# Performance work log

Measured on AMD Instinct MI355X. Metric: run time of the kernel, lower is better.

## Reference

```python
import jax, jax.numpy as jnp
import numpy as np

B = 8192          # batch
LATENT = 32       # latent_dim
H = 64            # hidden_size
SEQ_LEN = 180
NUM_CLASSES = 6
IN = 2            # GRU input size (zeros) / output features


def setup_inputs() -> dict:
    key = jax.random.key(0)
    ks = jax.random.split(key, 12)
    s_fc = 1.0 / np.sqrt(LATENT + H)
    s_rnn = 1.0 / np.sqrt(H)
    return {
        "z": jax.random.normal(ks[0], (B, LATENT), dtype=jnp.float32),
        "labels": jax.random.randint(ks[1], (B,), 0, NUM_CLASSES),
        "embed_w": jax.random.normal(ks[2], (NUM_CLASSES, H), dtype=jnp.float32),
        "fc_w": jax.random.uniform(ks[3], (H, LATENT + H), jnp.float32, -s_fc, s_fc),
        "fc_b": jax.random.uniform(ks[4], (H,), jnp.float32, -s_fc, s_fc),
        "w_ih": jax.random.uniform(ks[5], (3 * H, IN), jnp.float32, -s_rnn, s_rnn),
        "w_hh": jax.random.uniform(ks[6], (3 * H, H), jnp.float32, -s_rnn, s_rnn),
        "b_ih": jax.random.uniform(ks[7], (3 * H,), jnp.float32, -s_rnn, s_rnn),
        "b_hh": jax.random.uniform(ks[8], (3 * H,), jnp.float32, -s_rnn, s_rnn),
        "out_w": jax.random.uniform(ks[9], (IN, H), jnp.float32, -s_rnn, s_rnn),
        "out_b": jax.random.uniform(ks[10], (IN,), jnp.float32, -s_rnn, s_rnn),
    }


def reference(z, labels, embed_w, fc_w, fc_b, w_ih, w_hh, b_ih, b_hh, out_w, out_b):
    # h0 = tanh(fc([z, embed(labels)]))  -> [B, H]
    cond = embed_w[labels]
    h0 = jnp.tanh(jnp.concatenate([z, cond], axis=1) @ fc_w.T + fc_b)

    # GRU input is all zeros, so the input-side gates are constant per step:
    # gi = x_t @ w_ih.T + b_ih = b_ih  (kept faithful to torch GRU math)
    i_r, i_z, i_n = jnp.split(b_ih, 3)

    def step(h, _):
        gh = h @ w_hh.T + b_hh                      # [B, 3H]
        h_r, h_z, h_n = jnp.split(gh, 3, axis=-1)
        r = jax.nn.sigmoid(i_r + h_r)
        zg = jax.nn.sigmoid(i_z + h_z)
        n = jnp.tanh(i_n + r * h_n)
        h_new = (1.0 - zg) * n + zg * h
        return h_new, h_new

    _, hs = jax.lax.scan(step, h0, None, length=SEQ_LEN)  # [S, B, H]
    # out linear: [B, S, 2]
    return jnp.einsum("sbh,oh->bso", hs, out_w) + out_b
```

## Files before the change

### kernel.cpp

```cpp
#include <hip/hip_runtime.h>

#define NB     8192
#define HDIM   64
#define SEQ    180
#define MT     16
#define SB     72
#define XSP    100

typedef __bf16 bf16x8 __attribute__((ext_vector_type(8)));
typedef __bf16 bf16x4 __attribute__((ext_vector_type(4)));
typedef float  f32x4  __attribute__((ext_vector_type(4)));

#define L2E 1.44269504088896340736f

__device__ __forceinline__ float tanh_f(float x) {
    float e = __builtin_amdgcn_exp2f((2.0f * L2E) * x);
    return 1.0f - 2.0f * __builtin_amdgcn_rcpf(1.0f + e);
}

#define MFMA __builtin_amdgcn_mfma_f32_16x16x32_bf16

__global__ __launch_bounds__(256) void gru_all(
        const float* __restrict__ z, const int* __restrict__ labels,
        const float* __restrict__ embed_w, const float* __restrict__ fc_w,
        const float* __restrict__ fc_b, const float* __restrict__ w_hh,
        const float* __restrict__ b_ih, const float* __restrict__ b_hh,
        const float* __restrict__ out_w, const float* __restrict__ out_b,
        float* __restrict__ out) {
    __shared__ __align__(16) __bf16 hbuf[2][MT * SB];
    __shared__ __align__(16) float  xs[MT * XSP];

    const int t = threadIdx.x;
    const int w = t >> 6;
    const int l = t & 63;
    const int q = l >> 4;
    const int n16 = l & 15;
    const int jg = 16 * w + n16;
    const int jb = 16 * w + 4 * q;
    const int bbase = blockIdx.x * MT;

    for (int c = t; c < MT * 24; c += 256) {
        int m = c / 24, kk = (c % 24) * 4;
        f32x4 v;
        if (kk < 32) v = *(const f32x4*)(z + (size_t)(bbase + m) * 32 + kk);
        else         v = *(const f32x4*)(embed_w + labels[bbase + m] * 64 + (kk - 32));
        *(f32x4*)(xs + m * XSP + kk) = v;
    }

    bf16x8 whi[3][2];
#pragma unroll
    for (int g = 0; g < 3; ++g) {
        const float* pr = w_hh + (g * 64 + jg) * HDIM;
#pragma unroll
        for (int ks = 0; ks < 2; ++ks) {
            const float* p = pr + ks * 32 + q * 8;
            f32x4 va = *(const f32x4*)(p);
            f32x4 vb = *(const f32x4*)(p + 4);
#pragma unroll
            for (int j2 = 0; j2 < 4; ++j2) {
                whi[g][ks][j2]     = (__bf16)va[j2];
                whi[g][ks][4 + j2] = (__bf16)vb[j2];
            }
        }
    }

    bf16x8 obhi[2];
#pragma unroll
    for (int ks = 0; ks < 2; ++ks) {
        f32x4 va = {0.f, 0.f, 0.f, 0.f}, vb = {0.f, 0.f, 0.f, 0.f};
        if (n16 < 2) {
            va = *(const f32x4*)(out_w + n16 * 64 + ks * 32 + q * 8);
            vb = *(const f32x4*)(out_w + n16 * 64 + ks * 32 + q * 8 + 4);
        }
#pragma unroll
        for (int j2 = 0; j2 < 4; ++j2) {
            obhi[ks][j2]     = (__bf16)va[j2];
            obhi[ks][4 + j2] = (__bf16)vb[j2];
        }
    }
    const f32x4 obias = (q == 0) ? f32x4{out_b[0], out_b[1], 0.f, 0.f}
                                 : f32x4{0.f, 0.f, 0.f, 0.f};
    const f32x4 kZ = {0.f, 0.f, 0.f, 0.f};
    const f32x4 one4 = {1.f, 1.f, 1.f, 1.f};

    const bool ostorer = (q == 0) && ((n16 >> 2) == w);

    const f32x4 bihR = *(const f32x4*)(b_ih + jb);
    const f32x4 bhhR = *(const f32x4*)(b_hh + jb);
    const f32x4 bihZ = *(const f32x4*)(b_ih + 64 + jb);
    const f32x4 bhhZ = *(const f32x4*)(b_hh + 64 + jb);
    const f32x4 cR4 = (bihR + bhhR) * (-L2E);
    const f32x4 cZ4 = (bihZ + bhhZ) * (-L2E);
    const f32x4 bn4 = *(const f32x4*)(b_hh + 128 + jb);
    const f32x4 cN4 = (*(const f32x4*)(b_ih + 128 + jb)) * (2.0f * L2E);

    const int rdoff = n16 * SB + q * 8;
    const int wboff = n16 * SB + jb;
    float* opb = out + (size_t)(bbase + n16) * (SEQ * 2);

    __syncthreads();

    f32x4 hprev;
    {
        f32x4 a = *(const f32x4*)(fc_b + jb);
        for (int kc = 0; kc < 24; ++kc) {
            f32x4 xv = *(const f32x4*)(xs + n16 * XSP + kc * 4);
#pragma unroll
            for (int r = 0; r < 4; ++r) {
                f32x4 wv = *(const f32x4*)(fc_w + (size_t)(jb + r) * 96 + kc * 4);
                a[r] += wv[0] * xv[0] + wv[1] * xv[1] + wv[2] * xv[2] + wv[3] * xv[3];
            }
        }
        bf16x4 hp;
#pragma unroll
        for (int r = 0; r < 4; ++r) {
            hprev[r] = tanh_f(a[r]);
            hp[r] = (__bf16)hprev[r];
        }
        *(bf16x4*)(hbuf[0] + wboff) = hp;
    }
    __syncthreads();

    if ((blockIdx.x >> 8) & 1) __builtin_amdgcn_s_sleep(8);

    for (int u = 0; u < SEQ / 4; ++u) {
#pragma unroll
        for (int s = 0; s < 4; ++s) {
            const int p = s & 1;
            const __bf16* Hh = hbuf[p];
            __bf16* Nh = hbuf[1 - p];

            bf16x8 b0 = *(const bf16x8*)(Hh + rdoff);
            bf16x8 b1 = *(const bf16x8*)(Hh + rdoff + 32);

            f32x4 aR, aZ, aN;
            aR = MFMA(whi[0][0], b0, kZ, 0, 0, 0);
            aZ = MFMA(whi[1][0], b0, kZ, 0, 0, 0);
            aN = MFMA(whi[2][0], b0, kZ, 0, 0, 0);
            aR = MFMA(whi[0][1], b1, aR, 0, 0, 0);
            aZ = MFMA(whi[1][1], b1, aZ, 0, 0, 0);
            aN = MFMA(whi[2][1], b1, aN, 0, 0, 0);

            f32x4 tR = aR * (-L2E) + cR4;
            f32x4 tZ = aZ * (-L2E) + cZ4;
            f32x4 eR, eZ;
#pragma unroll
            for (int r = 0; r < 4; ++r) {
                eR[r] = __builtin_amdgcn_exp2f(tR[r]);
                eZ[r] = __builtin_amdgcn_exp2f(tZ[r]);
            }
            eR = eR + one4;
            eZ = eZ + one4;
            f32x4 rg, zg;
#pragma unroll
            for (int r = 0; r < 4; ++r) {
                rg[r] = __builtin_amdgcn_rcpf(eR[r]);
                zg[r] = __builtin_amdgcn_rcpf(eZ[r]);
            }
            f32x4 mm = aN + bn4;
            f32x4 tN = (rg * mm) * (2.0f * L2E) + cN4;
            f32x4 eN;
#pragma unroll
            for (int r = 0; r < 4; ++r) eN[r] = __builtin_amdgcn_exp2f(tN[r]);
            eN = eN + one4;
            f32x4 dd;
#pragma unroll
            for (int r = 0; r < 4; ++r) dd[r] = __builtin_amdgcn_rcpf(eN[r]);
            f32x4 ng = dd * (-2.0f) + one4;
            f32x4 hn = zg * (hprev - ng) + ng;
            hprev = hn;
            bf16x4 hp;
#pragma unroll
            for (int r = 0; r < 4; ++r) hp[r] = (__bf16)hn[r];
            *(bf16x4*)(Nh + wboff) = hp;

            {
                f32x4 o = obias;
                o = MFMA(obhi[0], b0, o, 0, 0, 0);
                o = MFMA(obhi[1], b1, o, 0, 0, 0);
                if ((u | s) != 0 && ostorer)
                    *(float2*)(opb + (8 * u + 2 * s - 2)) = make_float2(o[0], o[1]);
            }

            __syncthreads();
        }
    }

    {
        const __bf16* Hh = hbuf[0];
        bf16x8 b0 = *(const bf16x8*)(Hh + rdoff);
        bf16x8 b1 = *(const bf16x8*)(Hh + rdoff + 32);
        f32x4 o = obias;
        o = MFMA(obhi[0], b0, o, 0, 0, 0);
        o = MFMA(obhi[1], b1, o, 0, 0, 0);
        if (ostorer)
            *(float2*)(opb + (SEQ - 1) * 2) = make_float2(o[0], o[1]);
    }
}

extern "C" void kernel_launch(void* const* d_in, const int* in_sizes, int n_in,
                              void* d_out, int out_size, void* d_ws, size_t ws_size,
                              hipStream_t stream) {
    (void)in_sizes; (void)n_in; (void)out_size; (void)d_ws; (void)ws_size;
    const float* z       = (const float*)d_in[0];
    const int*   labels  = (const int*)d_in[1];
    const float* embed_w = (const float*)d_in[2];
    const float* fc_w    = (const float*)d_in[3];
    const float* fc_b    = (const float*)d_in[4];
    const float* w_hh    = (const float*)d_in[6];
    const float* b_ih    = (const float*)d_in[7];
    const float* b_hh    = (const float*)d_in[8];
    const float* out_w   = (const float*)d_in[9];
    const float* out_b   = (const float*)d_in[10];
    float* out = (float*)d_out;

    gru_all<<<NB / MT, 256, 0, stream>>>(z, labels, embed_w, fc_w, fc_b,
                                         w_hh, b_ih, b_hh, out_w, out_b, out);
}
```

Before: 172.7 us.

## Interleave two independent batch tiles per block to hide recurrence latency

Each block now processes two 16-row batch tiles, issuing the MFMAs and gate epilogues for both recurrences together so one tile's latency hides behind the other's work. This halves the grid and the number of per-step barriers per batch row. The blockIdx-based s_sleep stagger is removed. In exchange, register pressure rises and each CU gets fewer blocks, so less parallelism comes from separate wavefronts.

```diff
diff --git a/kernel.cpp b/kernel.cpp
--- a/kernel.cpp
+++ b/kernel.cpp
@@ -1,9 +1,10 @@
 #include <hip/hip_runtime.h>
 
-#define NB     8192
+#define NBATCH 8192
 #define HDIM   64
 #define SEQ    180
 #define MT     16
+#define NC     2
 #define SB     72
 #define XSP    100
 
@@ -19,6 +20,43 @@
 }
 
 #define MFMA __builtin_amdgcn_mfma_f32_16x16x32_bf16
+
+__device__ __forceinline__ f32x4 gru_epi(f32x4 aR, f32x4 aZ, f32x4 aN,
+        f32x4 cR4, f32x4 cZ4, f32x4 bn4, f32x4 cN4, f32x4 one4,
+        f32x4 hprev, __bf16* Nh, int wboff) {
+    f32x4 tR = aR * (-L2E) + cR4;
+    f32x4 tZ = aZ * (-L2E) + cZ4;
+    f32x4 eR, eZ;
+#pragma unroll
+    for (int r = 0; r < 4; ++r) {
+        eR[r] = __builtin_amdgcn_exp2f(tR[r]);
+        eZ[r] = __builtin_amdgcn_exp2f(tZ[r]);
+    }
+    eR = eR + one4;
+    eZ = eZ + one4;
+    f32x4 rg, zg;
+#pragma unroll
+    for (int r = 0; r < 4; ++r) {
+        rg[r] = __builtin_amdgcn_rcpf(eR[r]);
+        zg[r] = __builtin_amdgcn_rcpf(eZ[r]);
+    }
+    f32x4 mm = aN + bn4;
+    f32x4 tN = (rg * mm) * (2.0f * L2E) + cN4;
+    f32x4 eN;
+#pragma unroll
+    for (int r = 0; r < 4; ++r) eN[r] = __builtin_amdgcn_exp2f(tN[r]);
+    eN = eN + one4;
+    f32x4 dd;
+#pragma unroll
+    for (int r = 0; r < 4; ++r) dd[r] = __builtin_amdgcn_rcpf(eN[r]);
+    f32x4 ng = dd * (-2.0f) + one4;
+    f32x4 hn = zg * (hprev - ng) + ng;
+    bf16x4 hp;
+#pragma unroll
+    for (int r = 0; r < 4; ++r) hp[r] = (__bf16)hn[r];
+    *(bf16x4*)(Nh + wboff) = hp;
+    return hn;
+}
 
 __global__ __launch_bounds__(256) void gru_all(
         const float* __restrict__ z, const int* __restrict__ labels,
@@ -27,8 +65,8 @@
         const float* __restrict__ b_ih, const float* __restrict__ b_hh,
         const float* __restrict__ out_w, const float* __restrict__ out_b,
         float* __restrict__ out) {
-    __shared__ __align__(16) __bf16 hbuf[2][MT * SB];
-    __shared__ __align__(16) float  xs[MT * XSP];
+    __shared__ __align__(16) __bf16 hbuf[NC][2][MT * SB];
+    __shared__ __align__(16) float  xs[NC * MT * XSP];
 
     const int t = threadIdx.x;
     const int w = t >> 6;
@@ -37,9 +75,9 @@
     const int n16 = l & 15;
     const int jg = 16 * w + n16;
     const int jb = 16 * w + 4 * q;
-    const int bbase = blockIdx.x * MT;
-
-    for (int c = t; c < MT * 24; c += 256) {
+    const int bbase = blockIdx.x * (NC * MT);
+
+    for (int c = t; c < NC * MT * 24; c += 256) {
         int m = c / 24, kk = (c % 24) * 4;
         f32x4 v;
         if (kk < 32) v = *(const f32x4*)(z + (size_t)(bbase + m) * 32 + kk);
@@ -96,105 +134,97 @@
 
     const int rdoff = n16 * SB + q * 8;
     const int wboff = n16 * SB + jb;
-    float* opb = out + (size_t)(bbase + n16) * (SEQ * 2);
+    float* opbA = out + (size_t)(bbase + n16) * (SEQ * 2);
+    float* opbB = out + (size_t)(bbase + MT + n16) * (SEQ * 2);
 
     __syncthreads();
 
-    f32x4 hprev;
+    f32x4 hpA, hpB;
     {
-        f32x4 a = *(const f32x4*)(fc_b + jb);
+        f32x4 aA = *(const f32x4*)(fc_b + jb);
+        f32x4 aB = aA;
         for (int kc = 0; kc < 24; ++kc) {
-            f32x4 xv = *(const f32x4*)(xs + n16 * XSP + kc * 4);
+            f32x4 xvA = *(const f32x4*)(xs + n16 * XSP + kc * 4);
+            f32x4 xvB = *(const f32x4*)(xs + (MT + n16) * XSP + kc * 4);
 #pragma unroll
             for (int r = 0; r < 4; ++r) {
                 f32x4 wv = *(const f32x4*)(fc_w + (size_t)(jb + r) * 96 + kc * 4);
-                a[r] += wv[0] * xv[0] + wv[1] * xv[1] + wv[2] * xv[2] + wv[3] * xv[3];
+                aA[r] += wv[0] * xvA[0] + wv[1] * xvA[1] + wv[2] * xvA[2] + wv[3] * xvA[3];
+                aB[r] += wv[0] * xvB[0] + wv[1] * xvB[1] + wv[2] * xvB[2] + wv[3] * xvB[3];
             }
         }
-        bf16x4 hp;
+        bf16x4 ha, hb;
 #pragma unroll
         for (int r = 0; r < 4; ++r) {
-            hprev[r] = tanh_f(a[r]);
-            hp[r] = (__bf16)hprev[r];
-        }
-        *(bf16x4*)(hbuf[0] + wboff) = hp;
+            hpA[r] = tanh_f(aA[r]); ha[r] = (__bf16)hpA[r];
+            hpB[r] = tanh_f(aB[r]); hb[r] = (__bf16)hpB[r];
+        }
+        *(bf16x4*)(hbuf[0][0] + wboff) = ha;
+        *(bf16x4*)(hbuf[1][0] + wboff) = hb;
     }
     __syncthreads();
 
-    if ((blockIdx.x >> 8) & 1) __builtin_amdgcn_s_sleep(8);
-
-    for (int u = 0; u < SEQ / 4; ++u) {
-#pragma unroll
-        for (int s = 0; s < 4; ++s) {
-            const int p = s & 1;
-            const __bf16* Hh = hbuf[p];
-            __bf16* Nh = hbuf[1 - p];
-
-            bf16x8 b0 = *(const bf16x8*)(Hh + rdoff);
-            bf16x8 b1 = *(const bf16x8*)(Hh + rdoff + 32);
-
-            f32x4 aR, aZ, aN;
-            aR = MFMA(whi[0][0], b0, kZ, 0, 0, 0);
-            aZ = MFMA(whi[1][0], b0, kZ, 0, 0, 0);
-            aN = MFMA(whi[2][0], b0, kZ, 0, 0, 0);
-            aR = MFMA(whi[0][1], b1, aR, 0, 0, 0);
-            aZ = MFMA(whi[1][1], b1, aZ, 0, 0, 0);
-            aN = MFMA(whi[2][1], b1, aN, 0, 0, 0);
-
-            f32x4 tR = aR * (-L2E) + cR4;
-            f32x4 tZ = aZ * (-L2E) + cZ4;
-            f32x4 eR, eZ;
-#pragma unroll
-            for (int r = 0; r < 4; ++r) {
-                eR[r] = __builtin_amdgcn_exp2f(tR[r]);
-                eZ[r] = __builtin_amdgcn_exp2f(tZ[r]);
+    for (int u = 0; u < SEQ / 2; ++u) {
+#pragma unroll
+        for (int s = 0; s < 2; ++s) {
+            const __bf16* HA = hbuf[0][s];
+            __bf16*       NA = hbuf[0][s ^ 1];
+            const __bf16* HB = hbuf[1][s];
+            __bf16*      NhB = hbuf[1][s ^ 1];
+
+            bf16x8 a0 = *(const bf16x8*)(HA + rdoff);
+            bf16x8 a1 = *(const bf16x8*)(HA + rdoff + 32);
+            bf16x8 c0 = *(const bf16x8*)(HB + rdoff);
+            bf16x8 c1 = *(const bf16x8*)(HB + rdoff + 32);
+
+            f32x4 ArA = MFMA(whi[0][0], a0, kZ, 0, 0, 0);
+            f32x4 AzA = MFMA(whi[1][0], a0, kZ, 0, 0, 0);
+            f32x4 AnA = MFMA(whi[2][0], a0, kZ, 0, 0, 0);
+            f32x4 ArB = MFMA(whi[0][0], c0, kZ, 0, 0, 0);
+            f32x4 AzB = MFMA(whi[1][0], c0, kZ, 0, 0, 0);
+            f32x4 AnB = MFMA(whi[2][0], c0, kZ, 0, 0, 0);
+            ArA = MFMA(whi[0][1], a1, ArA, 0, 0, 0);
+            AzA = MFMA(whi[1][1], a1, AzA, 0, 0, 0);
+            AnA = MFMA(whi[2][1], a1, AnA, 0, 0, 0);
+            ArB = MFMA(whi[0][1], c1, ArB, 0, 0, 0);
+            AzB = MFMA(whi[1][1], c1, AzB, 0, 0, 0);
+            AnB = MFMA(whi[2][1], c1, AnB, 0, 0, 0);
+
+            {
+                f32x4 oA = obias;
+                oA = MFMA(obhi[0], a0, oA, 0, 0, 0);
+                oA = MFMA(obhi[1], a1, oA, 0, 0, 0);
+                f32x4 oB = obias;
+                oB = MFMA(obhi[0], c0, oB, 0, 0, 0);
+                oB = MFMA(obhi[1], c1, oB, 0, 0, 0);
+                if ((u | s) != 0 && ostorer) {
+                    *(float2*)(opbA + (4 * u + 2 * s - 2)) = make_float2(oA[0], oA[1]);
+                    *(float2*)(opbB + (4 * u + 2 * s - 2)) = make_float2(oB[0], oB[1]);
+                }
             }
-            eR = eR + one4;
-            eZ = eZ + one4;
-            f32x4 rg, zg;
-#pragma unroll
-            for (int r = 0; r < 4; ++r) {
-                rg[r] = __builtin_amdgcn_rcpf(eR[r]);
-                zg[r] = __builtin_amdgcn_rcpf(eZ[r]);
-            }
-            f32x4 mm = aN + bn4;
-            f32x4 tN = (rg * mm) * (2.0f * L2E) + cN4;
-            f32x4 eN;
-#pragma unroll
-            for (int r = 0; r < 4; ++r) eN[r] = __builtin_amdgcn_exp2f(tN[r]);
-            eN = eN + one4;
-            f32x4 dd;
-#pragma unroll
-            for (int r = 0; r < 4; ++r) dd[r] = __builtin_amdgcn_rcpf(eN[r]);
-            f32x4 ng = dd * (-2.0f) + one4;
-            f32x4 hn = zg * (hprev - ng) + ng;
-            hprev = hn;
-            bf16x4 hp;
-#pragma unroll
-            for (int r = 0; r < 4; ++r) hp[r] = (__bf16)hn[r];
-            *(bf16x4*)(Nh + wboff) = hp;
-
-            {
-                f32x4 o = obias;
-                o = MFMA(obhi[0], b0, o, 0, 0, 0);
-                o = MFMA(obhi[1], b1, o, 0, 0, 0);
-                if ((u | s) != 0 && ostorer)
-                    *(float2*)(opb + (8 * u + 2 * s - 2)) = make_float2(o[0], o[1]);
-            }
+
+            hpA = gru_epi(ArA, AzA, AnA, cR4, cZ4, bn4, cN4, one4, hpA, NA,  wboff);
+            hpB = gru_epi(ArB, AzB, AnB, cR4, cZ4, bn4, cN4, one4, hpB, NhB, wboff);
 
             __syncthreads();
         }
     }
 
     {
-        const __bf16* Hh = hbuf[0];
-        bf16x8 b0 = *(const bf16x8*)(Hh + rdoff);
-        bf16x8 b1 = *(const bf16x8*)(Hh + rdoff + 32);
-        f32x4 o = obias;
-        o = MFMA(obhi[0], b0, o, 0, 0, 0);
-        o = MFMA(obhi[1], b1, o, 0, 0, 0);
-        if (ostorer)
-            *(float2*)(opb + (SEQ - 1) * 2) = make_float2(o[0], o[1]);
+        bf16x8 a0 = *(const bf16x8*)(hbuf[0][0] + rdoff);
+        bf16x8 a1 = *(const bf16x8*)(hbuf[0][0] + rdoff + 32);
+        bf16x8 c0 = *(const bf16x8*)(hbuf[1][0] + rdoff);
+        bf16x8 c1 = *(const bf16x8*)(hbuf[1][0] + rdoff + 32);
+        f32x4 oA = obias;
+        oA = MFMA(obhi[0], a0, oA, 0, 0, 0);
+        oA = MFMA(obhi[1], a1, oA, 0, 0, 0);
+        f32x4 oB = obias;
+        oB = MFMA(obhi[0], c0, oB, 0, 0, 0);
+        oB = MFMA(obhi[1], c1, oB, 0, 0, 0);
+        if (ostorer) {
+            *(float2*)(opbA + (SEQ - 1) * 2) = make_float2(oA[0], oA[1]);
+            *(float2*)(opbB + (SEQ - 1) * 2) = make_float2(oB[0], oB[1]);
+        }
     }
 }
 
@@ -214,6 +244,6 @@
     const float* out_b   = (const float*)d_in[10];
     float* out = (float*)d_out;
 
-    gru_all<<<NB / MT, 256, 0, stream>>>(z, labels, embed_w, fc_w, fc_b,
-                                         w_hh, b_ih, b_hh, out_w, out_b, out);
-}
+    gru_all<<<NBATCH / (NC * MT), 256, 0, stream>>>(z, labels, embed_w, fc_w, fc_b,
+                                                    w_hh, b_ih, b_hh, out_w, out_b, out);
+}
```

After: 189.9 us. 1.1x slower.
